# Performance work log

Hardware: AMD Instinct MI355X
Metric: run time of the kernel (lower is better)

The kernel has to match this reference:

```python
import jax, jax.numpy as jnp
import numpy as np

TAU = 2.0          # LIF membrane time constant (spikingjelly default)
V_TH = 1.0         # v_threshold
V_RESET = 0.0      # hard reset value
ATAN_ALPHA = 2.0   # surrogate.ATan default alpha
EPS = 1e-12        # F.normalize eps

@jax.custom_vjp
def spike_fn(x):
    # Heaviside forward, ATan surrogate backward
    return (x >= 0).astype(x.dtype)

def _spike_fwd(x):
    return spike_fn(x), x

def _spike_bwd(x, g):
    sg = (ATAN_ALPHA / 2.0) / (1.0 + (jnp.pi / 2.0 * ATAN_ALPHA * x) ** 2)
    return (g * sg,)

spike_fn.defvjp(_spike_fwd, _spike_bwd)

def setup_inputs() -> dict:
    key = jax.random.key(0)
    k1, k2 = jax.random.split(key)
    T, B, F, H = 32, 512, 2048, 2048
    x_seq = jax.random.normal(k1, (T, B, F), dtype=jnp.float32)
    lim = float(np.sqrt(6.0 / (F + H)))  # xavier_uniform
    W = jax.random.uniform(k2, (H, F), dtype=jnp.float32, minval=-lim, maxval=lim)
    b = jnp.zeros((H,), dtype=jnp.float32)
    return {"x_seq": x_seq, "W": W, "b": b}

def reference(x_seq, W, b):
    # Linear: [T,B,F] @ [F,H] -> [T,B,H]
    cur = jnp.einsum('tbf,hf->tbh', x_seq, W) + b
    # F.normalize(dim=-1): L2 normalize the injected current per neuron vector
    norm = jnp.maximum(jnp.sqrt(jnp.sum(cur * cur, axis=-1, keepdims=True)), EPS)
    cur = cur / norm

    def step(v, c):
        # LIF charge: v <- v + (x - (v - v_reset)) / tau
        v = v + (c - (v - V_RESET)) / TAU
        s = spike_fn(v - V_TH)
        sd = jax.lax.stop_gradient(s)  # detach_reset=True
        v = v * (1.0 - sd) + V_RESET * sd  # hard reset
        return v, s

    v0 = jnp.zeros(cur.shape[1:], dtype=cur.dtype)  # [B,H]
    _, spk_seq = jax.lax.scan(step, v0, cur)  # spk_seq: [T,B,H]
    count = spk_seq.sum(axis=0)  # [B,H]
    return spk_seq, count
```

## Files before the change

kernel.cpp:

```cpp
#include <hip/hip_runtime.h>
#include <hip/hip_bf16.h>

#define T_SZ 32
#define B_SZ 512
#define F_SZ 2048
#define H_SZ 2048
#define M_SZ (T_SZ * B_SZ)

#define BM 128
#define BN 128
#define BK 128

typedef int   i32x8  __attribute__((ext_vector_type(8)));
typedef float f32x16 __attribute__((ext_vector_type(16)));
typedef unsigned short u16x8 __attribute__((ext_vector_type(8)));

__device__ __forceinline__ void gload_lds16(const void* g, void* l) {
    __builtin_amdgcn_global_load_lds(
        (const __attribute__((address_space(1))) unsigned int*)g,
        (__attribute__((address_space(3))) unsigned int*)l,
        16, 0, 0);
}

__device__ __forceinline__ float bf16_bits_to_f32(unsigned short u) {
    return __uint_as_float(((unsigned)u) << 16);
}

__global__ __launch_bounds__(256) void cvt_fp8_kernel(const float* __restrict__ in,
                                                      unsigned int* __restrict__ out,
                                                      float scale, int n8) {
    int i = blockIdx.x * 256 + threadIdx.x;
    if (i >= n8) return;
    float4 v0 = ((const float4*)in)[2 * i];
    float4 v1 = ((const float4*)in)[2 * i + 1];
    int w0 = __builtin_amdgcn_cvt_pk_fp8_f32(v0.x * scale, v0.y * scale, 0, false);
    w0     = __builtin_amdgcn_cvt_pk_fp8_f32(v0.z * scale, v0.w * scale, w0, true);
    int w1 = __builtin_amdgcn_cvt_pk_fp8_f32(v1.x * scale, v1.y * scale, 0, false);
    w1     = __builtin_amdgcn_cvt_pk_fp8_f32(v1.z * scale, v1.w * scale, w1, true);
    ((uint2*)out)[i] = make_uint2((unsigned)w0, (unsigned)w1);
}

__global__ __launch_bounds__(256) void init_ss_kernel(float4* __restrict__ ss4) {
    ss4[blockIdx.x * 256 + threadIdx.x] = make_float4(0.f, 0.f, 0.f, 0.f);
}

__global__ __launch_bounds__(256, 3) void gemm_fp8_kernel(const unsigned char* __restrict__ A,
                                                          const unsigned char* __restrict__ Bt,
                                                          const float* __restrict__ bias,
                                                          __hip_bfloat16* __restrict__ C,
                                                          float* __restrict__ ss)
{
    __shared__ __align__(16) unsigned char As[BM * BK];
    __shared__ __align__(16) unsigned char Bs[BN * BK];

    const int tid  = threadIdx.x;
    const int lane = tid & 63;
    const int wave = tid >> 6;
    const int wm   = wave >> 1;
    const int wn   = wave & 1;
    const int m0   = blockIdx.y * BM;
    const int n0   = blockIdx.x * BN;
    const int l31  = lane & 31;
    const int kh   = lane >> 5;

    f32x16 acc[2][2] = {};

    for (int k0 = 0; k0 < F_SZ; k0 += BK) {
        __syncthreads();
        #pragma unroll
        for (int j = 0; j < 4; ++j) {
            int c   = j * 256 + tid;
            int row = c >> 3;
            int u   = (c & 7) ^ (row & 7);
            gload_lds16(A + (size_t)(m0 + row) * F_SZ + k0 + u * 16, (void*)(As + c * 16));
        }
        #pragma unroll
        for (int j = 0; j < 4; ++j) {
            int c   = j * 256 + tid;
            int row = c >> 3;
            int u   = (c & 7) ^ (row & 7);
            gload_lds16(Bt + (size_t)(n0 + row) * F_SZ + k0 + u * 16, (void*)(Bs + c * 16));
        }
        __syncthreads();

        #pragma unroll
        for (int s = 0; s < 2; ++s) {
            i32x8 af[2], bq[2];
            #pragma unroll
            for (int i = 0; i < 2; ++i) {
                const int ra = wm * 64 + i * 32 + l31;
                const int rb = wn * 64 + i * 32 + l31;
                const int ua = s * 4 + kh * 2;
                ((int4*)&af[i])[0] = *(const int4*)(As + ra * BK + (((ua + 0) ^ (ra & 7)) * 16));
                ((int4*)&af[i])[1] = *(const int4*)(As + ra * BK + (((ua + 1) ^ (ra & 7)) * 16));
                ((int4*)&bq[i])[0] = *(const int4*)(Bs + rb * BK + (((ua + 0) ^ (rb & 7)) * 16));
                ((int4*)&bq[i])[1] = *(const int4*)(Bs + rb * BK + (((ua + 1) ^ (rb & 7)) * 16));
            }
            #pragma unroll
            for (int mi = 0; mi < 2; ++mi)
                #pragma unroll
                for (int ni = 0; ni < 2; ++ni)
                    acc[mi][ni] = __builtin_amdgcn_mfma_scale_f32_32x32x64_f8f6f4(
                        af[mi], bq[ni], acc[mi][ni],
                        0 , 0 ,
                        0, 0x7f7f7f7f,
                        0, 0x7f7f7f7f);
        }
    }

    float ssl[2][16];
    #pragma unroll
    for (int ni = 0; ni < 2; ++ni) {
        const int gn = n0 + wn * 64 + ni * 32 + l31;
        const float bv = bias[gn];
        #pragma unroll
        for (int mi = 0; mi < 2; ++mi) {
            const int gmb = m0 + wm * 64 + mi * 32 + 4 * kh;
            #pragma unroll
            for (int r = 0; r < 16; ++r) {
                const int grow = gmb + (r & 3) + 8 * (r >> 2);
                const float val = acc[mi][ni][r] * (1.0f / 256.0f) + bv;
                C[(size_t)grow * H_SZ + gn] = __float2bfloat16(val);
                if (ni == 0) ssl[mi][r] = val * val;
                else         ssl[mi][r] += val * val;
            }
        }
    }
    #pragma unroll
    for (int mi = 0; mi < 2; ++mi) {
        const int gmb = m0 + wm * 64 + mi * 32 + 4 * kh;
        #pragma unroll
        for (int r = 0; r < 16; ++r) {
            float p = ssl[mi][r];
            p += __shfl_xor(p, 1, 64);
            p += __shfl_xor(p, 2, 64);
            p += __shfl_xor(p, 4, 64);
            p += __shfl_xor(p, 8, 64);
            p += __shfl_xor(p, 16, 64);
            if (l31 == 0)
                atomicAdd(ss + gmb + (r & 3) + 8 * (r >> 2), p);
        }
    }
}

__global__ __launch_bounds__(256) void lif_scan_kernel(const __hip_bfloat16* __restrict__ cur,
                                                       const float* __restrict__ ss,
                                                       float* __restrict__ spk,
                                                       float* __restrict__ cnt)
{
    const int gid = blockIdx.x * 256 + threadIdx.x;
    const int b   = gid >> 9;
    const int h0  = (gid & 511) * 4;

    float v[4]  = {0, 0, 0, 0};
    float cn[4] = {0, 0, 0, 0};
    #pragma unroll
    for (int t = 0; t < T_SZ; ++t) {
        const size_t off = (size_t)(t * B_SZ + b) * H_SZ + h0;
        const ushort4 pk = *(const ushort4*)(cur + off);
        const float inv  = 1.0f / fmaxf(sqrtf(ss[t * B_SZ + b]), 1e-12f);
        float so[4];
        {
            float c;
            c = bf16_bits_to_f32(pk.x) * inv; v[0] += (c - v[0]) * 0.5f;
            c = bf16_bits_to_f32(pk.y) * inv; v[1] += (c - v[1]) * 0.5f;
            c = bf16_bits_to_f32(pk.z) * inv; v[2] += (c - v[2]) * 0.5f;
            c = bf16_bits_to_f32(pk.w) * inv; v[3] += (c - v[3]) * 0.5f;
        }
        #pragma unroll
        for (int j = 0; j < 4; ++j) {
            float s = (v[j] >= 1.0f) ? 1.0f : 0.0f;
            so[j] = s;
            cn[j] += s;
            v[j] = (s != 0.f) ? 0.f : v[j];
        }
        *(float4*)(spk + off) = make_float4(so[0], so[1], so[2], so[3]);
    }
    *(float4*)(cnt + (size_t)b * H_SZ + h0) = make_float4(cn[0], cn[1], cn[2], cn[3]);
}

extern "C" void kernel_launch(void* const* d_in, const int* in_sizes, int n_in,
                              void* d_out, int out_size, void* d_ws, size_t ws_size,
                              hipStream_t stream) {
    const float* x    = (const float*)d_in[0];
    const float* W    = (const float*)d_in[1];
    const float* bias = (const float*)d_in[2];

    float* spk = (float*)d_out;
    float* cnt = spk + (size_t)T_SZ * B_SZ * H_SZ;

    char* ws = (char*)d_ws;
    unsigned char* x8    = (unsigned char*)ws;
    unsigned char* W8    = x8 + (size_t)M_SZ * F_SZ;
    __hip_bfloat16* curb = (__hip_bfloat16*)(W8 + (size_t)H_SZ * F_SZ);
    float* ss            = (float*)((char*)curb + (size_t)M_SZ * H_SZ * 2);

    init_ss_kernel<<<M_SZ / 1024, 256, 0, stream>>>((float4*)ss);
    cvt_fp8_kernel<<<(M_SZ * F_SZ / 8) / 256, 256, 0, stream>>>(x, (unsigned int*)x8, 1.0f,   M_SZ * F_SZ / 8);
    cvt_fp8_kernel<<<(H_SZ * F_SZ / 8) / 256, 256, 0, stream>>>(W, (unsigned int*)W8, 256.0f, H_SZ * F_SZ / 8);
    gemm_fp8_kernel<<<dim3(H_SZ / BN, M_SZ / BM), 256, 0, stream>>>(x8, W8, bias, curb, ss);
    lif_scan_kernel<<<(B_SZ * H_SZ / 4) / 256, 256, 0, stream>>>(curb, ss, spk, cnt);
}
```

Before: 355.2 us.

## Store GEMM output as fp8, halve K tile, and merge prep kernels

The intermediate current tensor is now stored as fp8 instead of bf16, which halves the GEMM write traffic and the scan read traffic. BK drops from 128 to 64 with a new LDS swizzle, and launch bounds no longer request 3 blocks per CU. The two conversion kernels and the ss init are merged into one prep kernel to cut launch overhead. Storing the current as fp8 costs precision and can flip spikes near threshold. The GEMM now does a byte-wide scattered store per element.

New measurement: 360.5 us. No clear change (+1.5%).

```diff
diff --git a/kernel.cpp b/kernel.cpp
--- a/kernel.cpp
+++ b/kernel.cpp
@@ -9,11 +9,11 @@
 
 #define BM 128
 #define BN 128
-#define BK 128
+#define BK 64
 
 typedef int   i32x8  __attribute__((ext_vector_type(8)));
 typedef float f32x16 __attribute__((ext_vector_type(16)));
-typedef unsigned short u16x8 __attribute__((ext_vector_type(8)));
+typedef float f32x2  __attribute__((ext_vector_type(2)));
 
 __device__ __forceinline__ void gload_lds16(const void* g, void* l) {
     __builtin_amdgcn_global_load_lds(
@@ -22,33 +22,37 @@
         16, 0, 0);
 }
 
-__device__ __forceinline__ float bf16_bits_to_f32(unsigned short u) {
-    return __uint_as_float(((unsigned)u) << 16);
+__global__ __launch_bounds__(256) void prep_kernel(const float* __restrict__ x,
+                                                   const float* __restrict__ W,
+                                                   unsigned int* __restrict__ x8,
+                                                   unsigned int* __restrict__ W8,
+                                                   float4* __restrict__ ss4) {
+    const int bid = blockIdx.x;
+    const int tid = threadIdx.x;
+    if (bid < 18432) {
+        const float* in;
+        unsigned int* out;
+        float scale;
+        int i;
+        if (bid < 16384) { in = x; out = x8; scale = 1.0f;   i = bid * 256 + tid; }
+        else             { in = W; out = W8; scale = 256.0f; i = (bid - 16384) * 256 + tid; }
+        float4 v0 = ((const float4*)in)[2 * i];
+        float4 v1 = ((const float4*)in)[2 * i + 1];
+        int w0 = __builtin_amdgcn_cvt_pk_fp8_f32(v0.x * scale, v0.y * scale, 0, false);
+        w0     = __builtin_amdgcn_cvt_pk_fp8_f32(v0.z * scale, v0.w * scale, w0, true);
+        int w1 = __builtin_amdgcn_cvt_pk_fp8_f32(v1.x * scale, v1.y * scale, 0, false);
+        w1     = __builtin_amdgcn_cvt_pk_fp8_f32(v1.z * scale, v1.w * scale, w1, true);
+        ((uint2*)out)[i] = make_uint2((unsigned)w0, (unsigned)w1);
+    } else {
+        ss4[(bid - 18432) * 256 + tid] = make_float4(0.f, 0.f, 0.f, 0.f);
+    }
 }
 
-__global__ __launch_bounds__(256) void cvt_fp8_kernel(const float* __restrict__ in,
-                                                      unsigned int* __restrict__ out,
-                                                      float scale, int n8) {
-    int i = blockIdx.x * 256 + threadIdx.x;
-    if (i >= n8) return;
-    float4 v0 = ((const float4*)in)[2 * i];
-    float4 v1 = ((const float4*)in)[2 * i + 1];
-    int w0 = __builtin_amdgcn_cvt_pk_fp8_f32(v0.x * scale, v0.y * scale, 0, false);
-    w0     = __builtin_amdgcn_cvt_pk_fp8_f32(v0.z * scale, v0.w * scale, w0, true);
-    int w1 = __builtin_amdgcn_cvt_pk_fp8_f32(v1.x * scale, v1.y * scale, 0, false);
-    w1     = __builtin_amdgcn_cvt_pk_fp8_f32(v1.z * scale, v1.w * scale, w1, true);
-    ((uint2*)out)[i] = make_uint2((unsigned)w0, (unsigned)w1);
-}
-
-__global__ __launch_bounds__(256) void init_ss_kernel(float4* __restrict__ ss4) {
-    ss4[blockIdx.x * 256 + threadIdx.x] = make_float4(0.f, 0.f, 0.f, 0.f);
-}
-
-__global__ __launch_bounds__(256, 3) void gemm_fp8_kernel(const unsigned char* __restrict__ A,
-                                                          const unsigned char* __restrict__ Bt,
-                                                          const float* __restrict__ bias,
-                                                          __hip_bfloat16* __restrict__ C,
-                                                          float* __restrict__ ss)
+__global__ __launch_bounds__(256) void gemm_fp8_kernel(const unsigned char* __restrict__ A,
+                                                       const unsigned char* __restrict__ Bt,
+                                                       const float* __restrict__ bias,
+                                                       unsigned char* __restrict__ C8,
+                                                       float* __restrict__ ss)
 {
     __shared__ __align__(16) unsigned char As[BM * BK];
     __shared__ __align__(16) unsigned char Bs[BN * BK];
@@ -68,44 +72,36 @@
     for (int k0 = 0; k0 < F_SZ; k0 += BK) {
         __syncthreads();
         #pragma unroll
-        for (int j = 0; j < 4; ++j) {
+        for (int j = 0; j < 2; ++j) {
             int c   = j * 256 + tid;
-            int row = c >> 3;
-            int u   = (c & 7) ^ (row & 7);
-            gload_lds16(A + (size_t)(m0 + row) * F_SZ + k0 + u * 16, (void*)(As + c * 16));
-        }
-        #pragma unroll
-        for (int j = 0; j < 4; ++j) {
-            int c   = j * 256 + tid;
-            int row = c >> 3;
-            int u   = (c & 7) ^ (row & 7);
+            int row = c >> 2;
+            int u   = (c & 3) ^ ((row >> 1) & 3);
+            gload_lds16(A  + (size_t)(m0 + row) * F_SZ + k0 + u * 16, (void*)(As + c * 16));
             gload_lds16(Bt + (size_t)(n0 + row) * F_SZ + k0 + u * 16, (void*)(Bs + c * 16));
         }
         __syncthreads();
 
+        i32x8 af[2], bq[2];
         #pragma unroll
-        for (int s = 0; s < 2; ++s) {
-            i32x8 af[2], bq[2];
+        for (int i = 0; i < 2; ++i) {
+            const int ra = wm * 64 + i * 32 + l31;
+            const int rb = wn * 64 + i * 32 + l31;
+            const int sa = (ra >> 1) & 3;
+            const int sb = (rb >> 1) & 3;
+            ((int4*)&af[i])[0] = *(const int4*)(As + ra * 64 + (((kh * 2 + 0) ^ sa) * 16));
+            ((int4*)&af[i])[1] = *(const int4*)(As + ra * 64 + (((kh * 2 + 1) ^ sa) * 16));
+            ((int4*)&bq[i])[0] = *(const int4*)(Bs + rb * 64 + (((kh * 2 + 0) ^ sb) * 16));
+            ((int4*)&bq[i])[1] = *(const int4*)(Bs + rb * 64 + (((kh * 2 + 1) ^ sb) * 16));
+        }
+        #pragma unroll
+        for (int mi = 0; mi < 2; ++mi)
             #pragma unroll
-            for (int i = 0; i < 2; ++i) {
-                const int ra = wm * 64 + i * 32 + l31;
-                const int rb = wn * 64 + i * 32 + l31;
-                const int ua = s * 4 + kh * 2;
-                ((int4*)&af[i])[0] = *(const int4*)(As + ra * BK + (((ua + 0) ^ (ra & 7)) * 16));
-                ((int4*)&af[i])[1] = *(const int4*)(As + ra * BK + (((ua + 1) ^ (ra & 7)) * 16));
-                ((int4*)&bq[i])[0] = *(const int4*)(Bs + rb * BK + (((ua + 0) ^ (rb & 7)) * 16));
-                ((int4*)&bq[i])[1] = *(const int4*)(Bs + rb * BK + (((ua + 1) ^ (rb & 7)) * 16));
-            }
-            #pragma unroll
-            for (int mi = 0; mi < 2; ++mi)
-                #pragma unroll
-                for (int ni = 0; ni < 2; ++ni)
-                    acc[mi][ni] = __builtin_amdgcn_mfma_scale_f32_32x32x64_f8f6f4(
-                        af[mi], bq[ni], acc[mi][ni],
-                        0 , 0 ,
-                        0, 0x7f7f7f7f,
-                        0, 0x7f7f7f7f);
-        }
+            for (int ni = 0; ni < 2; ++ni)
+                acc[mi][ni] = __builtin_amdgcn_mfma_scale_f32_32x32x64_f8f6f4(
+                    af[mi], bq[ni], acc[mi][ni],
+                    0 , 0 ,
+                    0, 0x7f7f7f7f,
+                    0, 0x7f7f7f7f);
     }
 
     float ssl[2][16];
@@ -120,7 +116,8 @@
             for (int r = 0; r < 16; ++r) {
                 const int grow = gmb + (r & 3) + 8 * (r >> 2);
                 const float val = acc[mi][ni][r] * (1.0f / 256.0f) + bv;
-                C[(size_t)grow * H_SZ + gn] = __float2bfloat16(val);
+                const int p = __builtin_amdgcn_cvt_pk_fp8_f32(val, val, 0, false);
+                C8[(size_t)grow * H_SZ + gn] = (unsigned char)(p & 0xff);
                 if (ni == 0) ssl[mi][r] = val * val;
                 else         ssl[mi][r] += val * val;
             }
@@ -143,7 +140,7 @@
     }
 }
 
-__global__ __launch_bounds__(256) void lif_scan_kernel(const __hip_bfloat16* __restrict__ cur,
+__global__ __launch_bounds__(256) void lif_scan_kernel(const unsigned char* __restrict__ cur8,
                                                        const float* __restrict__ ss,
                                                        float* __restrict__ spk,
                                                        float* __restrict__ cnt)
@@ -157,16 +154,16 @@
     #pragma unroll
     for (int t = 0; t < T_SZ; ++t) {
         const size_t off = (size_t)(t * B_SZ + b) * H_SZ + h0;
-        const ushort4 pk = *(const ushort4*)(cur + off);
-        const float inv  = 1.0f / fmaxf(sqrtf(ss[t * B_SZ + b]), 1e-12f);
+        const unsigned int w = *(const unsigned int*)(cur8 + off);
+        const float inv = 1.0f / fmaxf(sqrtf(ss[t * B_SZ + b]), 1e-12f);
+        const f32x2 lo = __builtin_amdgcn_cvt_pk_f32_fp8(w, false);
+        const f32x2 hi = __builtin_amdgcn_cvt_pk_f32_fp8(w, true);
+        float c0 = lo[0] * inv, c1 = lo[1] * inv, c2 = hi[0] * inv, c3 = hi[1] * inv;
+        v[0] += (c0 - v[0]) * 0.5f;
+        v[1] += (c1 - v[1]) * 0.5f;
+        v[2] += (c2 - v[2]) * 0.5f;
+        v[3] += (c3 - v[3]) * 0.5f;
         float so[4];
-        {
-            float c;
-            c = bf16_bits_to_f32(pk.x) * inv; v[0] += (c - v[0]) * 0.5f;
-            c = bf16_bits_to_f32(pk.y) * inv; v[1] += (c - v[1]) * 0.5f;
-            c = bf16_bits_to_f32(pk.z) * inv; v[2] += (c - v[2]) * 0.5f;
-            c = bf16_bits_to_f32(pk.w) * inv; v[3] += (c - v[3]) * 0.5f;
-        }
         #pragma unroll
         for (int j = 0; j < 4; ++j) {
             float s = (v[j] >= 1.0f) ? 1.0f : 0.0f;
@@ -192,12 +189,10 @@
     char* ws = (char*)d_ws;
     unsigned char* x8    = (unsigned char*)ws;
     unsigned char* W8    = x8 + (size_t)M_SZ * F_SZ;
-    __hip_bfloat16* curb = (__hip_bfloat16*)(W8 + (size_t)H_SZ * F_SZ);
-    float* ss            = (float*)((char*)curb + (size_t)M_SZ * H_SZ * 2);
+    unsigned char* cur8  = W8 + (size_t)H_SZ * F_SZ;
+    float* ss            = (float*)(cur8 + (size_t)M_SZ * H_SZ);
 
-    init_ss_kernel<<<M_SZ / 1024, 256, 0, stream>>>((float4*)ss);
-    cvt_fp8_kernel<<<(M_SZ * F_SZ / 8) / 256, 256, 0, stream>>>(x, (unsigned int*)x8, 1.0f,   M_SZ * F_SZ / 8);
-    cvt_fp8_kernel<<<(H_SZ * F_SZ / 8) / 256, 256, 0, stream>>>(W, (unsigned int*)W8, 256.0f, H_SZ * F_SZ / 8);
-    gemm_fp8_kernel<<<dim3(H_SZ / BN, M_SZ / BM), 256, 0, stream>>>(x8, W8, bias, curb, ss);
-    lif_scan_kernel<<<(B_SZ * H_SZ / 4) / 256, 256, 0, stream>>>(curb, ss, spk, cnt);
+    prep_kernel<<<18448, 256, 0, stream>>>(x, W, (unsigned int*)x8, (unsigned int*)W8, (float4*)ss);
+    gemm_fp8_kernel<<<dim3(H_SZ / BN, M_SZ / BM), 256, 0, stream>>>(x8, W8, bias, cur8, ss);
+    lif_scan_kernel<<<(B_SZ * H_SZ / 4) / 256, 256, 0, stream>>>(cur8, ss, spk, cnt);
 }
```
